# Performance work log

Measured on AMD Instinct MI355X. Metric: run time of the kernel, lower is better.

Reference implementation:

```python
import jax, jax.numpy as jnp
import numpy as np
from math import sqrt

D_MODEL = 1024
N_HEADS = 16
D_V = D_MODEL // N_HEADS
D_FF = 4 * D_MODEL
EPS = 1e-5


def setup_inputs() -> dict:
    key = jax.random.key(0)
    ks = jax.random.split(key, 12)
    N, L = 2, 2048
    s = 0.02
    return {
        'queries': jax.random.normal(ks[0], (N, L, D_MODEL), jnp.float32),
        'keys': jax.random.normal(ks[1], (N, L, D_MODEL), jnp.float32),
        'values': jax.random.normal(ks[2], (N, L, D_MODEL), jnp.float32),
        'mask': jnp.ones((N, 1, 1, L), jnp.int32),
        'fc_w': jax.random.normal(ks[3], (D_MODEL, D_MODEL), jnp.float32) * s,
        'fc_b': jnp.zeros((D_MODEL,), jnp.float32),
        'ln1_g': jnp.ones((D_MODEL,), jnp.float32),
        'ln1_b': jnp.zeros((D_MODEL,), jnp.float32),
        'ff_w1': jax.random.normal(ks[4], (D_MODEL, D_FF), jnp.float32) * s,
        'ff_b1': jnp.zeros((D_FF,), jnp.float32),
        'ff_w2': jax.random.normal(ks[5], (D_FF, D_MODEL), jnp.float32) * s,
        'ff_b2': jnp.zeros((D_MODEL,), jnp.float32),
        'ln2_g': jnp.ones((D_MODEL,), jnp.float32),
        'ln2_b': jnp.zeros((D_MODEL,), jnp.float32),
    }


def layer_norm(x, g, b):
    mu = jnp.mean(x, axis=-1, keepdims=True)
    var = jnp.mean(jnp.square(x - mu), axis=-1, keepdims=True)
    return (x - mu) * jax.lax.rsqrt(var + EPS) * g + b


def reference(queries, keys, values, mask, fc_w, fc_b, ln1_g, ln1_b,
              ff_w1, ff_b1, ff_w2, ff_b2, ln2_g, ln2_b):
    N, Lq, _ = queries.shape
    Lk = keys.shape[1]
    # NOTE: the original module never applies its Q/K/V linear layers; raw
    # inputs are reshaped directly into heads.
    q = queries.reshape(N, Lq, N_HEADS, D_V).transpose(0, 2, 1, 3)  # nhqd
    k = keys.reshape(N, Lk, N_HEADS, D_V)                           # nlhd
    v = values.reshape(N, Lk, N_HEADS, D_V)                         # nlhd
    energy = jnp.einsum('nhqd,nlhd->nhql', q, k)
    energy = jnp.where(mask == 0, -jnp.inf, energy)
    # original scales by sqrt(d_model), not sqrt(d_v)
    attn = jax.nn.softmax(energy / sqrt(D_MODEL), axis=-1)
    out = jnp.einsum('nhql,nlhd->nqhd', attn, v).reshape(N, Lq, D_MODEL)
    attention = out @ fc_w + fc_b
    x1 = layer_norm(attention + queries, ln1_g, ln1_b)
    fc = jax.nn.relu(x1 @ ff_w1 + ff_b1) @ ff_w2 + ff_b2
    x2 = layer_norm(fc + x1, ln2_g, ln2_b)
    return x2
```

## Files before the change

### kernel.cpp

```cpp
#include <hip/hip_runtime.h>
#include <stdint.h>

typedef unsigned short u16;
typedef __bf16 bf16x8 __attribute__((ext_vector_type(8), may_alias));
typedef float f32x4 __attribute__((ext_vector_type(4), may_alias));

typedef void __attribute__((address_space(1))) as1_void;
typedef void __attribute__((address_space(3))) as3_void;

#define MFMA16 __builtin_amdgcn_mfma_f32_16x16x32_bf16

#define SBAR()                                \
    do {                                      \
        asm volatile("" ::: "memory");        \
        __builtin_amdgcn_s_barrier();         \
        asm volatile("" ::: "memory");        \
    } while (0)
#define WAITV(n) asm volatile("s_waitcnt vmcnt(" #n ")" ::: "memory")
#define WAITL0() asm volatile("s_waitcnt lgkmcnt(0)" ::: "memory")

__device__ __forceinline__ void async_copy16(const void* g, void* l) {
    __builtin_amdgcn_global_load_lds((as1_void*)g, (as3_void*)l, 16, 0, 0);
}

__device__ __forceinline__ u16 f2bf(float f) {
    union { float f; unsigned u; } c; c.f = f;
    unsigned u = c.u;
    u += 0x7fffu + ((u >> 16) & 1u);
    return (u16)(u >> 16);
}
__device__ __forceinline__ float bf2f(u16 u) {
    return __uint_as_float((unsigned)u << 16);
}

__global__ __launch_bounds__(256) void prep_all(
    const float* __restrict__ q, u16* __restrict__ qbf, float qscale,
    const float* __restrict__ k, u16* __restrict__ kbf,
    const float* __restrict__ v, u16* __restrict__ vT,
    const float* __restrict__ fcw, u16* __restrict__ fcwT,
    const float* __restrict__ w1, u16* __restrict__ w1T,
    const float* __restrict__ w2, u16* __restrict__ w2T) {
    __shared__ float tile[64][65];
    int g = blockIdx.x;
    int t = threadIdx.x;
    if (g >= 3328) {
        g -= 3328;
        const float* in;
        u16* out;
        float sc;
        if (g < 4096) { in = q; out = qbf; sc = qscale; }
        else { g -= 4096; in = k; out = kbf; sc = 1.0f; }
        size_t i = (size_t)g * 256 + t;
        f32x4 vv = *(const f32x4*)&in[i * 4];
        ushort4 o;
        o.x = f2bf(vv[0] * sc); o.y = f2bf(vv[1] * sc);
        o.z = f2bf(vv[2] * sc); o.w = f2bf(vv[3] * sc);
        *(ushort4*)&out[i * 4] = o;
        return;
    }
    const float* in;
    u16* out;
    int R, C, bx, by, bz = 0;
    if (g < 1024) { in = v; out = vT; R = 2048; C = 1024; bz = g >> 9; g &= 511; bx = g & 15; by = g >> 4; }
    else if (g < 1280) { g -= 1024; in = fcw; out = fcwT; R = 1024; C = 1024; bx = g & 15; by = g >> 4; }
    else if (g < 2304) { g -= 1280; in = w1; out = w1T; R = 1024; C = 4096; bx = g & 63; by = g >> 6; }
    else { g -= 2304; in = w2; out = w2T; R = 4096; C = 1024; bx = g & 15; by = g >> 4; }
    const float* inb = in + (size_t)bz * R * C;
    u16* outb = out + (size_t)bz * R * C;
    int c0 = bx * 64, r0 = by * 64;
    int tr = t >> 4, tc = (t & 15) * 4;
#pragma unroll
    for (int p = 0; p < 4; ++p) {
        int r = tr + p * 16;
        f32x4 vv = *(const f32x4*)&inb[(size_t)(r0 + r) * C + c0 + tc];
        tile[r][tc] = vv[0]; tile[r][tc + 1] = vv[1];
        tile[r][tc + 2] = vv[2]; tile[r][tc + 3] = vv[3];
    }
    __syncthreads();
    int wc = t >> 4, wr = (t & 15) * 4;
#pragma unroll
    for (int p = 0; p < 4; ++p) {
        int cl = wc + p * 16;
        ushort4 o;
        o.x = f2bf(tile[wr + 0][cl]); o.y = f2bf(tile[wr + 1][cl]);
        o.z = f2bf(tile[wr + 2][cl]); o.w = f2bf(tile[wr + 3][cl]);
        *(ushort4*)&outb[(size_t)(c0 + cl) * R + r0 + wr] = o;
    }
}

__global__ __launch_bounds__(256) void flash_attn(
    const u16* __restrict__ Q, const u16* __restrict__ Kb,
    const u16* __restrict__ VT, const int* __restrict__ mask,
    u16* __restrict__ O) {
    __shared__ u16 kls[2][8192];
    __shared__ u16 vls[8192];
    __shared__ u16 pls[8][2048];

    const int bid = blockIdx.x;
    const int qt = bid & 15;
    const int h = (bid >> 4) & 15;
    const int n = bid >> 8;
    const int t = threadIdx.x;
    const int w = t >> 6, lane = t & 63;
    const int m16 = lane & 15, quad = lane >> 4;

    const size_t qrowA = (size_t)(n * 2048 + qt * 128 + w * 16 + m16);
    const size_t qrowB = qrowA + 64;
    bf16x8 qfA0 = *(const bf16x8*)&Q[qrowA * 1024 + h * 64 + quad * 8];
    bf16x8 qfA1 = *(const bf16x8*)&Q[qrowA * 1024 + h * 64 + 32 + quad * 8];
    bf16x8 qfB0 = *(const bf16x8*)&Q[qrowB * 1024 + h * 64 + quad * 8];
    bf16x8 qfB1 = *(const bf16x8*)&Q[qrowB * 1024 + h * 64 + 32 + quad * 8];

    const int* maskn = mask + n * 2048;
    int allones;
    {
        int ok = 1;
#pragma unroll
        for (int i = 0; i < 8; ++i) {
            int4 mv = *(const int4*)&maskn[lane * 32 + i * 4];
            ok &= (mv.x != 0) & (mv.y != 0) & (mv.z != 0) & (mv.w != 0);
        }
        allones = __all(ok);
    }

    f32x4 otA[4] = {}, otB[4] = {};
    f32x4 sumA = {}, sumB = {};

    const u16* Kbase = Kb + (size_t)(n * 2048) * 1024 + h * 64;
    const u16* Vbase = VT + (size_t)(n * 1024 + h * 64) * 2048;
    u16* pwA = &pls[w * 2][0];
    u16* pwB = &pls[w * 2 + 1][0];

#pragma unroll
    for (int i = 0; i < 4; ++i) {
        int e = w * 4 + i;
        async_copy16(&Kbase[(size_t)((e >> 1) * 16 + m16) * 1024 + (e & 1) * 32 + quad * 8],
                     &kls[0][e * 512]);
    }
    __syncthreads();

    for (int kt = 0; kt < 16; ++kt) {
        const u16* kcur = kls[kt & 1];
        if (kt + 1 < 16) {
            u16* knext = kls[(kt + 1) & 1];
#pragma unroll
            for (int i = 0; i < 4; ++i) {
                int e = w * 4 + i;
                async_copy16(&Kbase[(size_t)((kt + 1) * 128 + (e >> 1) * 16 + m16) * 1024 +
                                    (e & 1) * 32 + quad * 8], &knext[e * 512]);
            }
        }
#pragma unroll
        for (int i = 0; i < 4; ++i) {
            int e = w * 4 + i;
            async_copy16(&Vbase[(size_t)((e >> 2) * 16 + m16) * 2048 + kt * 128 +
                                (e & 3) * 32 + quad * 8], &vls[e * 512]);
        }

        f32x4 sA[8] = {}, sB[8] = {};
#pragma unroll
        for (int ct = 0; ct < 8; ++ct) {
            bf16x8 a0 = *(const bf16x8*)&kcur[(ct * 2 + 0) * 512 + lane * 8];
            bf16x8 a1 = *(const bf16x8*)&kcur[(ct * 2 + 1) * 512 + lane * 8];
            sA[ct] = MFMA16(a0, qfA0, sA[ct], 0, 0, 0);
            sA[ct] = MFMA16(a1, qfA1, sA[ct], 0, 0, 0);
            sB[ct] = MFMA16(a0, qfB0, sB[ct], 0, 0, 0);
            sB[ct] = MFMA16(a1, qfB1, sB[ct], 0, 0, 0);
        }

        if (allones) {
#pragma unroll
            for (int ct = 0; ct < 8; ++ct) {
                int c = ct * 2 + (quad >> 1);
                int off = m16 * 128 + (((c ^ m16) & 15) << 3) + (quad & 1) * 4;
                {
                    float p0 = __builtin_amdgcn_exp2f(sA[ct][0]);
                    float p1 = __builtin_amdgcn_exp2f(sA[ct][1]);
                    float p2 = __builtin_amdgcn_exp2f(sA[ct][2]);
                    float p3 = __builtin_amdgcn_exp2f(sA[ct][3]);
                    sumA[0] += p0; sumA[1] += p1; sumA[2] += p2; sumA[3] += p3;
                    unsigned lo = __builtin_amdgcn_perm(__float_as_uint(p1), __float_as_uint(p0), 0x07060302);
                    unsigned hi = __builtin_amdgcn_perm(__float_as_uint(p3), __float_as_uint(p2), 0x07060302);
                    *(uint2*)&pwA[off] = make_uint2(lo, hi);
                }
                {
                    float p0 = __builtin_amdgcn_exp2f(sB[ct][0]);
                    float p1 = __builtin_amdgcn_exp2f(sB[ct][1]);
                    float p2 = __builtin_amdgcn_exp2f(sB[ct][2]);
                    float p3 = __builtin_amdgcn_exp2f(sB[ct][3]);
                    sumB[0] += p0; sumB[1] += p1; sumB[2] += p2; sumB[3] += p3;
                    unsigned lo = __builtin_amdgcn_perm(__float_as_uint(p1), __float_as_uint(p0), 0x07060302);
                    unsigned hi = __builtin_amdgcn_perm(__float_as_uint(p3), __float_as_uint(p2), 0x07060302);
                    *(uint2*)&pwB[off] = make_uint2(lo, hi);
                }
            }
        } else {
#pragma unroll
            for (int ct = 0; ct < 8; ++ct) {
                const int4 mv = *(const int4*)&maskn[kt * 128 + ct * 16 + quad * 4];
                int c = ct * 2 + (quad >> 1);
                int off = m16 * 128 + (((c ^ m16) & 15) << 3) + (quad & 1) * 4;
                {
                    float p0 = __builtin_amdgcn_exp2f(sA[ct][0]) * (mv.x ? 1.f : 0.f);
                    float p1 = __builtin_amdgcn_exp2f(sA[ct][1]) * (mv.y ? 1.f : 0.f);
                    float p2 = __builtin_amdgcn_exp2f(sA[ct][2]) * (mv.z ? 1.f : 0.f);
                    float p3 = __builtin_amdgcn_exp2f(sA[ct][3]) * (mv.w ? 1.f : 0.f);
                    sumA[0] += p0; sumA[1] += p1; sumA[2] += p2; sumA[3] += p3;
                    unsigned lo = __builtin_amdgcn_perm(__float_as_uint(p1), __float_as_uint(p0), 0x07060302);
                    unsigned hi = __builtin_amdgcn_perm(__float_as_uint(p3), __float_as_uint(p2), 0x07060302);
                    *(uint2*)&pwA[off] = make_uint2(lo, hi);
                }
                {
                    float p0 = __builtin_amdgcn_exp2f(sB[ct][0]) * (mv.x ? 1.f : 0.f);
                    float p1 = __builtin_amdgcn_exp2f(sB[ct][1]) * (mv.y ? 1.f : 0.f);
                    float p2 = __builtin_amdgcn_exp2f(sB[ct][2]) * (mv.z ? 1.f : 0.f);
                    float p3 = __builtin_amdgcn_exp2f(sB[ct][3]) * (mv.w ? 1.f : 0.f);
                    sumB[0] += p0; sumB[1] += p1; sumB[2] += p2; sumB[3] += p3;
                    unsigned lo = __builtin_amdgcn_perm(__float_as_uint(p1), __float_as_uint(p0), 0x07060302);
                    unsigned hi = __builtin_amdgcn_perm(__float_as_uint(p3), __float_as_uint(p2), 0x07060302);
                    *(uint2*)&pwB[off] = make_uint2(lo, hi);
                }
            }
        }

        __syncthreads();

        bf16x8 pfA[4], pfB[4];
#pragma unroll
        for (int kc2 = 0; kc2 < 4; ++kc2) {
            int off = m16 * 128 + ((((kc2 * 4 + quad) ^ m16) & 15) << 3);
            pfA[kc2] = *(const bf16x8*)&pwA[off];
            pfB[kc2] = *(const bf16x8*)&pwB[off];
        }
#pragma unroll
        for (int kc2 = 0; kc2 < 4; ++kc2) {
#pragma unroll
            for (int dt = 0; dt < 4; ++dt) {
                bf16x8 vf = *(const bf16x8*)&vls[(dt * 4 + kc2) * 512 + lane * 8];
                otA[dt] = MFMA16(vf, pfA[kc2], otA[dt], 0, 0, 0);
                otB[dt] = MFMA16(vf, pfB[kc2], otB[dt], 0, 0, 0);
            }
        }
        __syncthreads();
    }

    float lA = (sumA[0] + sumA[1]) + (sumA[2] + sumA[3]);
    float lB = (sumB[0] + sumB[1]) + (sumB[2] + sumB[3]);
    lA += __shfl_xor(lA, 16); lA += __shfl_xor(lA, 32);
    lB += __shfl_xor(lB, 16); lB += __shfl_xor(lB, 32);
    float invA = 1.f / fmaxf(lA, 1e-30f);
    float invB = 1.f / fmaxf(lB, 1e-30f);

    const size_t obA = qrowA * 1024 + h * 64;
    const size_t obB = qrowB * 1024 + h * 64;
#pragma unroll
    for (int dt = 0; dt < 4; ++dt) {
        unsigned lo = (unsigned)f2bf(otA[dt][0] * invA) | ((unsigned)f2bf(otA[dt][1] * invA) << 16);
        unsigned hi = (unsigned)f2bf(otA[dt][2] * invA) | ((unsigned)f2bf(otA[dt][3] * invA) << 16);
        *(uint2*)&O[obA + dt * 16 + quad * 4] = make_uint2(lo, hi);
        lo = (unsigned)f2bf(otB[dt][0] * invB) | ((unsigned)f2bf(otB[dt][1] * invB) << 16);
        hi = (unsigned)f2bf(otB[dt][2] * invB) | ((unsigned)f2bf(otB[dt][3] * invB) << 16);
        *(uint2*)&O[obB + dt * 16 + quad * 4] = make_uint2(lo, hi);
    }
}

template <int BM, int BN, int RELU, int OUTBF, int SPLITK>
__global__ __launch_bounds__(256) void gemm_bt(
    const u16* __restrict__ A, const u16* __restrict__ Bt,
    const float* __restrict__ bias, void* __restrict__ Cout,
    void* __restrict__ Cout1, int M, int N, int K) {
    constexpr int MI = BM / 32;
    constexpr int NJ = BN / 32;
    __shared__ u16 sm[2][(BM + BN) * 64];
    const int lane = threadIdx.x & 63;
    const int w = threadIdx.x >> 6;
    const int m16 = lane & 15, quad = lane >> 4;
    const int nBn = N / BN;
    int bid = blockIdx.x;
    int slice = 0;
    if (SPLITK > 1) {
        const int nblk = (M / BM) * nBn;
        slice = bid / nblk;
        bid = bid - slice * nblk;
    }
    const int bm = bid / nBn, bn = bid % nBn;
    const int r2 = w >> 1, c2 = w & 1;
    const int Ks = K / SPLITK;
    const int kOff = slice * Ks;

    const u16* Abase = A + (size_t)(bm * BM + m16) * K + quad * 8;
    const u16* Bbase = Bt + (size_t)(bn * BN + m16) * K + quad * 8;

    auto stage = [&](int buf, int k0) {
        u16* smA = &sm[buf][0];
        u16* smB = smA + BM * 64;
#pragma unroll
        for (int i = 0; i < MI; ++i) {
            int e = w * MI + i;
            async_copy16(&Abase[(size_t)((e >> 1) * 16) * K + k0 + (e & 1) * 32], &smA[e * 512]);
        }
#pragma unroll
        for (int i = 0; i < NJ; ++i) {
            int e = w * NJ + i;
            async_copy16(&Bbase[(size_t)((e >> 1) * 16) * K + k0 + (e & 1) * 32], &smB[e * 512]);
        }
    };

    f32x4 acc[MI][NJ] = {};
    const int nK = Ks >> 6;
    stage(0, kOff);
    __syncthreads();
    for (int kt = 0; kt < nK; ++kt) {
        if (kt + 1 < nK) stage((kt + 1) & 1, kOff + ((kt + 1) << 6));
        const u16* smA = &sm[kt & 1][0];
        const u16* smB = smA + BM * 64;
#pragma unroll
        for (int kc = 0; kc < 2; ++kc) {
            bf16x8 a[MI], b[NJ];
#pragma unroll
            for (int i = 0; i < MI; ++i)
                a[i] = *(const bf16x8*)&smA[((r2 * MI + i) * 2 + kc) * 512 + lane * 8];
#pragma unroll
            for (int j = 0; j < NJ; ++j)
                b[j] = *(const bf16x8*)&smB[((c2 * NJ + j) * 2 + kc) * 512 + lane * 8];
#pragma unroll
            for (int i = 0; i < MI; ++i)
#pragma unroll
                for (int j = 0; j < NJ; ++j)
                    acc[i][j] = MFMA16(a[i], b[j], acc[i][j], 0, 0, 0);
        }
        __syncthreads();
    }
    float bv[NJ];
#pragma unroll
    for (int j = 0; j < NJ; ++j)
        bv[j] = (SPLITK == 1 || slice == 0)
                    ? bias[bn * BN + c2 * (BN / 2) + j * 16 + m16] : 0.f;
    void* Csel = (SPLITK > 1 && slice != 0) ? Cout1 : Cout;
#pragma unroll
    for (int i = 0; i < MI; ++i) {
        int row0 = bm * BM + r2 * (BM / 2) + i * 16 + quad * 4;
#pragma unroll
        for (int j = 0; j < NJ; ++j) {
            int col = bn * BN + c2 * (BN / 2) + j * 16 + m16;
#pragma unroll
            for (int r = 0; r < 4; ++r) {
                float v = acc[i][j][r] + bv[j];
                if (RELU) v = fmaxf(v, 0.f);
                size_t idx = (size_t)(row0 + r) * N + col;
                if (OUTBF) ((u16*)Csel)[idx] = f2bf(v);
                else ((float*)Csel)[idx] = v;
            }
        }
    }
}

template <int RELU, int OUTBF>
__global__ __launch_bounds__(512, 2) void gemm_8ph(
    const u16* __restrict__ A, const u16* __restrict__ Bt,
    const float* __restrict__ bias, void* __restrict__ Cout,
    int M, int N, int K) {
    __shared__ u16 sm[2][2][16384];
    const int t = threadIdx.x;
    const int w = t >> 6, lane = t & 63;
    const int m16 = lane & 15, quad = lane >> 4;
    const int wm = w >> 2, wn = w & 3;
    const int nBn = N >> 8;
    const int bid = blockIdx.x;
    const int bm = bid / nBn, bn = bid % nBn;
    const int nK = K >> 6, nIter = nK >> 1;
    const u16* Abase = A + (size_t)(bm * 256 + m16) * K + quad * 8;
    const u16* Bbase = Bt + (size_t)(bn * 256 + m16) * K + quad * 8;

    auto stage_ht = [&](int kt, int part) {
        if (kt < nK) {
            const u16* base = (part < 2) ? Abase : Bbase;
            u16* lds = &sm[kt & 1][part >> 1][0];
#pragma unroll
            for (int i = 0; i < 2; ++i) {
                int e;
                if (part == 0)      e = i * 16 + w;
                else if (part == 1) e = 8 + i * 16 + w;
                else if (part == 2) e = i * 8 + w;
                else                e = 16 + i * 8 + w;
                async_copy16(&base[(size_t)((e >> 1) * 16) * K + (size_t)kt * 64 + (e & 1) * 32],
                             &lds[e * 512]);
            }
        }
    };
    auto ldsA = [&](int buf, int mf, int kc) {
        return *(const bf16x8*)&sm[buf][0][((wm * 8 + mf) * 2 + kc) * 512 + lane * 8];
    };
    auto ldsB = [&](int buf, int nf, int kc) {
        return *(const bf16x8*)&sm[buf][1][((wn * 4 + nf) * 2 + kc) * 512 + lane * 8];
    };

    f32x4 acc[8][4] = {};
    bf16x8 a0[4][2], a1[4][2], b[4][2];

#define QUAD8(Ar, BO, MO)                                                       \
    do {                                                                        \
        __builtin_amdgcn_s_setprio(1);                                          \
        _Pragma("unroll") for (int mi = 0; mi < 4; ++mi)                        \
            _Pragma("unroll") for (int nj = 0; nj < 2; ++nj)                    \
                _Pragma("unroll") for (int kc = 0; kc < 2; ++kc)                \
                    acc[(MO) + mi][(BO) + nj] =                                 \
                        MFMA16(Ar[mi][kc], b[(BO) + nj][kc],                    \
                               acc[(MO) + mi][(BO) + nj], 0, 0, 0);             \
        __builtin_amdgcn_s_setprio(0);                                          \
    } while (0)

    stage_ht(0, 0); stage_ht(0, 1); stage_ht(0, 2); stage_ht(0, 3);
    stage_ht(1, 0); stage_ht(1, 1); stage_ht(1, 2);
    WAITV(6);
    SBAR();

    for (int it = 0; it < nIter; ++it) {
        const int T1 = 2 * it + 1, T2 = 2 * it + 2, T3 = 2 * it + 3;
        const bool last = (it + 1 == nIter);
#pragma unroll
        for (int mf = 0; mf < 4; ++mf) { a0[mf][0] = ldsA(0, mf, 0); a0[mf][1] = ldsA(0, mf, 1); }
#pragma unroll
        for (int nf = 0; nf < 2; ++nf) { b[nf][0] = ldsB(0, nf, 0); b[nf][1] = ldsB(0, nf, 1); }
        stage_ht(T1, 3);
        SBAR(); WAITL0();
        QUAD8(a0, 0, 0);
        SBAR();
#pragma unroll
        for (int mf = 0; mf < 4; ++mf) { a1[mf][0] = ldsA(0, mf + 4, 0); a1[mf][1] = ldsA(0, mf + 4, 1); }
#pragma unroll
        for (int nf = 0; nf < 2; ++nf) { b[2 + nf][0] = ldsB(0, 2 + nf, 0); b[2 + nf][1] = ldsB(0, 2 + nf, 1); }
        stage_ht(T2, 0);
        SBAR(); WAITL0();
        QUAD8(a0, 2, 0);
        SBAR();
        stage_ht(T2, 1);
        SBAR(); WAITL0();
        QUAD8(a1, 2, 4);
        SBAR();
        stage_ht(T2, 2);
        if (last) { WAITV(0); } else { WAITV(6); }
        SBAR(); WAITL0();
        QUAD8(a1, 0, 4);
        SBAR();
#pragma unroll
        for (int mf = 0; mf < 4; ++mf) { a0[mf][0] = ldsA(1, mf, 0); a0[mf][1] = ldsA(1, mf, 1); }
#pragma unroll
        for (int nf = 0; nf < 2; ++nf) { b[nf][0] = ldsB(1, nf, 0); b[nf][1] = ldsB(1, nf, 1); }
        stage_ht(T2, 3);
        SBAR(); WAITL0();
        QUAD8(a0, 0, 0);
        SBAR();
#pragma unroll
        for (int mf = 0; mf < 4; ++mf) { a1[mf][0] = ldsA(1, mf + 4, 0); a1[mf][1] = ldsA(1, mf + 4, 1); }
#pragma unroll
        for (int nf = 0; nf < 2; ++nf) { b[2 + nf][0] = ldsB(1, 2 + nf, 0); b[2 + nf][1] = ldsB(1, 2 + nf, 1); }
        stage_ht(T3, 0);
        SBAR(); WAITL0();
        QUAD8(a0, 2, 0);
        SBAR();
        stage_ht(T3, 1);
        SBAR(); WAITL0();
        QUAD8(a1, 2, 4);
        SBAR();
        stage_ht(T3, 2);
        if (last) { WAITV(0); } else { WAITV(6); }
        SBAR(); WAITL0();
        QUAD8(a1, 0, 4);
        SBAR();
    }
#undef QUAD8

    float bv[4];
#pragma unroll
    for (int nf = 0; nf < 4; ++nf)
        bv[nf] = bias[bn * 256 + wn * 64 + nf * 16 + m16];
    const int colb = bn * 256 + wn * 64 + m16;
#pragma unroll
    for (int mf = 0; mf < 8; ++mf) {
        const int row0 = bm * 256 + wm * 128 + mf * 16 + quad * 4;
#pragma unroll
        for (int nf = 0; nf < 4; ++nf) {
#pragma unroll
            for (int r = 0; r < 4; ++r) {
                float vv = acc[mf][nf][r] + bv[nf];
                if (RELU) vv = fmaxf(vv, 0.f);
                size_t idx = (size_t)(row0 + r) * N + colb + nf * 16;
                if (OUTBF) ((u16*)Cout)[idx] = f2bf(vv);
                else ((float*)Cout)[idx] = vv;
            }
        }
    }
}

template <int RELU, int OUTBF, int SPLITK>
__global__ __launch_bounds__(512, 2) void gemm_sk(
    const u16* __restrict__ A, const u16* __restrict__ Bt,
    const float* __restrict__ bias,
    void* __restrict__ C0, void* __restrict__ C1,
    int M, int N, int K) {
    __shared__ u16 smA[2][8192];
    __shared__ u16 smB[2][16384];
    const int t = threadIdx.x;
    const int w = t >> 6, lane = t & 63;
    const int m16 = lane & 15, quad = lane >> 4;
    const int wm = w >> 2, wn = w & 3;
    const int nBn = N >> 8;
    const int nblk = (M >> 7) * nBn * SPLITK;
    const int o = blockIdx.x;
    const int v = (o & 7) * (nblk >> 3) + (o >> 3);
    const int gsz = nBn * SPLITK;
    const int bm = v / gsz;
    const int rr = v - bm * gsz;
    const int slice = rr / nBn;
    const int bn = rr - slice * nBn;
    const int Ks = K / SPLITK;
    const int nK = Ks >> 6, nIter = nK >> 1;
    const u16* Abase = A + (size_t)(bm * 128 + m16) * K + slice * Ks + quad * 8;
    const u16* Bbase = Bt + (size_t)(bn * 256 + m16) * K + slice * Ks + quad * 8;

    auto stage_u = [&](int kt, int part) {
        if (kt < nK) {
#pragma unroll
            for (int i = 0; i < 2; ++i) {
                const int idx = i * 8 + w;
                int e;
                const u16* base;
                u16* lds;
                if (part == 0) {
                    e = idx; base = Abase; lds = &smA[kt & 1][0];
                } else {
                    const int rbs = idx >> 1;
                    const int rb = ((rbs >> 1) << 2) | (rbs & 1) | ((part == 2) ? 2 : 0);
                    e = rb * 2 + (idx & 1);
                    base = Bbase; lds = &smB[kt & 1][0];
                }
                async_copy16(&base[(size_t)((e >> 1) * 16) * K + (size_t)kt * 64 + (e & 1) * 32],
                             &lds[e * 512]);
            }
        }
    };
    auto ldsA = [&](int buf, int mf, int kc) {
        return *(const bf16x8*)&smA[buf][((wm * 4 + mf) * 2 + kc) * 512 + lane * 8];
    };
    auto ldsB = [&](int buf, int nf, int kc) {
        return *(const bf16x8*)&smB[buf][((wn * 4 + nf) * 2 + kc) * 512 + lane * 8];
    };

    f32x4 acc[4][4] = {};
    bf16x8 af[4][2], bf[2][2];

#define QUADS(NO)                                                               \
    do {                                                                        \
        __builtin_amdgcn_s_setprio(1);                                          \
        _Pragma("unroll") for (int mi = 0; mi < 4; ++mi)                        \
            _Pragma("unroll") for (int nj = 0; nj < 2; ++nj)                    \
                _Pragma("unroll") for (int kc = 0; kc < 2; ++kc)                \
                    acc[mi][(NO) + nj] =                                        \
                        MFMA16(af[mi][kc], bf[nj][kc],                          \
                               acc[mi][(NO) + nj], 0, 0, 0);                    \
        __builtin_amdgcn_s_setprio(0);                                          \
    } while (0)

    stage_u(0, 0); stage_u(0, 1); stage_u(0, 2);
    stage_u(1, 0); stage_u(1, 1);
    WAITV(4);
    SBAR();

    for (int it = 0; it < nIter; ++it) {
        const int T1 = 2 * it + 1, T2 = 2 * it + 2, T3 = 2 * it + 3;
        const bool last = (it + 1 == nIter);
#pragma unroll
        for (int mf = 0; mf < 4; ++mf) { af[mf][0] = ldsA(0, mf, 0); af[mf][1] = ldsA(0, mf, 1); }
#pragma unroll
        for (int nf = 0; nf < 2; ++nf) { bf[nf][0] = ldsB(0, nf, 0); bf[nf][1] = ldsB(0, nf, 1); }
        stage_u(T1, 2);
        SBAR(); WAITL0();
        QUADS(0);
        SBAR();
#pragma unroll
        for (int nf = 0; nf < 2; ++nf) { bf[nf][0] = ldsB(0, 2 + nf, 0); bf[nf][1] = ldsB(0, 2 + nf, 1); }
        stage_u(T2, 0); stage_u(T2, 1);
        if (last) { WAITV(0); } else { WAITV(4); }
        SBAR(); WAITL0();
        QUADS(2);
        SBAR();
#pragma unroll
        for (int mf = 0; mf < 4; ++mf) { af[mf][0] = ldsA(1, mf, 0); af[mf][1] = ldsA(1, mf, 1); }
#pragma unroll
        for (int nf = 0; nf < 2; ++nf) { bf[nf][0] = ldsB(1, nf, 0); bf[nf][1] = ldsB(1, nf, 1); }
        stage_u(T2, 2);
        SBAR(); WAITL0();
        QUADS(0);
        SBAR();
#pragma unroll
        for (int nf = 0; nf < 2; ++nf) { bf[nf][0] = ldsB(1, 2 + nf, 0); bf[nf][1] = ldsB(1, 2 + nf, 1); }
        stage_u(T3, 0); stage_u(T3, 1);
        if (last) { WAITV(0); } else { WAITV(4); }
        SBAR(); WAITL0();
        QUADS(2);
        SBAR();
    }
#undef QUADS

    float bv[4];
#pragma unroll
    for (int nf = 0; nf < 4; ++nf)
        bv[nf] = (SPLITK == 1 || slice == 0)
                     ? bias[bn * 256 + wn * 64 + nf * 16 + m16] : 0.f;
    void* Csel = (SPLITK > 1 && slice != 0) ? C1 : C0;
    const int colb = bn * 256 + wn * 64 + m16;
#pragma unroll
    for (int mf = 0; mf < 4; ++mf) {
        const int row0 = bm * 128 + wm * 64 + mf * 16 + quad * 4;
#pragma unroll
        for (int nf = 0; nf < 4; ++nf) {
#pragma unroll
            for (int r = 0; r < 4; ++r) {
                float vv = acc[mf][nf][r] + bv[nf];
                if (RELU) vv = fmaxf(vv, 0.f);
                size_t idx = (size_t)(row0 + r) * N + colb + nf * 16;
                if (OUTBF) ((u16*)Csel)[idx] = f2bf(vv);
                else ((float*)Csel)[idx] = vv;
            }
        }
    }
}

template <int RESBF>
__global__ __launch_bounds__(256) void ln_residual(
    const float* __restrict__ x, const float* x2,
    const void* __restrict__ res,
    const float* __restrict__ g, const float* __restrict__ b,
    float* out_f32, u16* __restrict__ out_bf16) {
    __shared__ float smr[8];
    int row = blockIdx.x;
    int t = threadIdx.x;
    f32x4 xv = *(const f32x4*)&x[(size_t)row * 1024 + t * 4];
    f32x4 rv;
    if (RESBF) {
        ushort4 rb = *(const ushort4*)&((const u16*)res)[(size_t)row * 1024 + t * 4];
        rv[0] = bf2f(rb.x); rv[1] = bf2f(rb.y); rv[2] = bf2f(rb.z); rv[3] = bf2f(rb.w);
    } else {
        rv = *(const f32x4*)&((const float*)res)[(size_t)row * 1024 + t * 4];
    }
    xv += rv;
    if (x2) xv += *(const f32x4*)&x2[(size_t)row * 1024 + t * 4];
    float s = xv[0] + xv[1] + xv[2] + xv[3];
    float ss = xv[0] * xv[0] + xv[1] * xv[1] + xv[2] * xv[2] + xv[3] * xv[3];
#pragma unroll
    for (int d = 1; d < 64; d <<= 1) {
        s += __shfl_xor(s, d);
        ss += __shfl_xor(ss, d);
    }
    int w = t >> 6, lane = t & 63;
    if (lane == 0) { smr[w] = s; smr[4 + w] = ss; }
    __syncthreads();
    s = smr[0] + smr[1] + smr[2] + smr[3];
    ss = smr[4] + smr[5] + smr[6] + smr[7];
    float mu = s * (1.f / 1024.f);
    float var = ss * (1.f / 1024.f) - mu * mu;
    float rs = rsqrtf(var + 1e-5f);
    f32x4 gv = *(const f32x4*)&g[t * 4];
    f32x4 bv = *(const f32x4*)&b[t * 4];
    f32x4 y;
#pragma unroll
    for (int i = 0; i < 4; ++i) y[i] = (xv[i] - mu) * rs * gv[i] + bv[i];
    if (out_f32) *(f32x4*)&out_f32[(size_t)row * 1024 + t * 4] = y;
    if (out_bf16) {
        ushort4 o;
        o.x = f2bf(y[0]); o.y = f2bf(y[1]); o.z = f2bf(y[2]); o.w = f2bf(y[3]);
        *(ushort4*)&out_bf16[(size_t)row * 1024 + t * 4] = o;
    }
}

extern "C" void kernel_launch(void* const* d_in, const int* in_sizes, int n_in,
                              void* d_out, int out_size, void* d_ws, size_t ws_size,
                              hipStream_t stream) {
    const float* q = (const float*)d_in[0];
    const float* k = (const float*)d_in[1];
    const float* v = (const float*)d_in[2];
    const int* mask = (const int*)d_in[3];
    const float* fc_b = (const float*)d_in[5];
    const float* ln1_g = (const float*)d_in[6];
    const float* ln1_b = (const float*)d_in[7];
    const float* ff_b1 = (const float*)d_in[9];
    const float* ff_b2 = (const float*)d_in[11];
    const float* ln2_g = (const float*)d_in[12];
    const float* ln2_b = (const float*)d_in[13];
    const float* fc_w = (const float*)d_in[4];
    const float* ff_w1 = (const float*)d_in[8];
    const float* ff_w2 = (const float*)d_in[10];

    char* ws = (char*)d_ws;
    const size_t MB = 1024 * 1024;
    u16* qbf = (u16*)(ws + 0);
    u16* kbf = (u16*)(ws + 8 * MB);
    u16* vT  = (u16*)(ws + 16 * MB);
    u16* ao  = (u16*)(ws + 24 * MB);
    u16* hbuf = (u16*)(ws + 0);
    u16* fcwT = (u16*)(ws + 32 * MB);
    u16* w1T  = (u16*)(ws + 34 * MB);
    u16* w2T  = (u16*)(ws + 42 * MB);
    float* attn_raw = (float*)(ws + 50 * MB);
    float* fc_raw   = (float*)(ws + 50 * MB);
    u16* x1bf   = (u16*)(ws + 82 * MB);
    float* attn_rawB = (float*)(ws + 0);
    float* fcB  = (float*)(ws + 90 * MB);
    const bool big = ws_size >= 106 * MB;

    const float k2 = 0.03125f * 1.44269504088896340736f;

    prep_all<<<11520, 256, 0, stream>>>(q, qbf, k2, k, kbf, v, vT,
                                        fc_w, fcwT, ff_w1, w1T, ff_w2, w2T);

    flash_attn<<<512, 256, 0, stream>>>(qbf, kbf, vT, mask, ao);

    gemm_sk<0, 0, 2><<<256, 512, 0, stream>>>(
        ao, fcwT, fc_b, attn_raw, attn_rawB, 4096, 1024, 1024);
    ln_residual<0><<<4096, 256, 0, stream>>>(attn_raw, attn_rawB, q, ln1_g, ln1_b,
                                             nullptr, x1bf);

    gemm_8ph<1, 1><<<256, 512, 0, stream>>>(
        x1bf, w1T, ff_b1, hbuf, 4096, 4096, 1024);

    if (big) {
        gemm_sk<0, 0, 2><<<256, 512, 0, stream>>>(
            hbuf, w2T, ff_b2, fc_raw, fcB, 4096, 1024, 4096);
        ln_residual<1><<<4096, 256, 0, stream>>>(fc_raw, fcB, x1bf, ln2_g, ln2_b,
                                                 (float*)d_out, (u16*)nullptr);
    } else {
        gemm_bt<64, 128, 0, 0, 1><<<64 * 8, 256, 0, stream>>>(
            hbuf, w2T, ff_b2, fc_raw, nullptr, 4096, 1024, 4096);
        ln_residual<1><<<4096, 256, 0, stream>>>(fc_raw, nullptr, x1bf, ln2_g, ln2_b,
                                                 (float*)d_out, (u16*)nullptr);
    }
}
```

Baseline: 350.9 us.

## Restructure GEMM main loops to overlap LDS reads with MFMA and coalesce bf16 stores

Rewrites the barrier and wait schedule in both GEMM kernels. Fragment reads from LDS are now issued before the MFMA clusters without an immediate lgkmcnt(0) wait, and B fragments are double-registered so the next reads overlap the current math. This removes about half the barriers per iteration. The bf16 epilogue of the large GEMM now stages results through LDS and writes 16-byte coalesced rows instead of scattered 2-byte stores. The main risk is correctness if the reduced waits let LDS buffers be overwritten or read too early.

```diff
diff --git a/kernel.cpp b/kernel.cpp
--- a/kernel.cpp
+++ b/kernel.cpp
@@ -17,7 +17,7 @@
         asm volatile("" ::: "memory");        \
     } while (0)
 #define WAITV(n) asm volatile("s_waitcnt vmcnt(" #n ")" ::: "memory")
-#define WAITL0() asm volatile("s_waitcnt lgkmcnt(0)" ::: "memory")
+#define WAITL(n) asm volatile("s_waitcnt lgkmcnt(" #n ")" ::: "memory")
 
 __device__ __forceinline__ void async_copy16(const void* g, void* l) {
     __builtin_amdgcn_global_load_lds((as1_void*)g, (as3_void*)l, 16, 0, 0);
@@ -396,98 +396,115 @@
     };
 
     f32x4 acc[8][4] = {};
-    bf16x8 a0[4][2], a1[4][2], b[4][2];
-
-#define QUAD8(Ar, BO, MO)                                                       \
+    bf16x8 a0[4][2], a1[4][2], b01[2][2], b23[2][2];
+
+#define RD_A0(buf)                                                              \
+    _Pragma("unroll") for (int mf = 0; mf < 4; ++mf) {                          \
+        a0[mf][0] = ldsA(buf, mf, 0); a0[mf][1] = ldsA(buf, mf, 1); }
+#define RD_A1(buf)                                                              \
+    _Pragma("unroll") for (int mf = 0; mf < 4; ++mf) {                          \
+        a1[mf][0] = ldsA(buf, mf + 4, 0); a1[mf][1] = ldsA(buf, mf + 4, 1); }
+#define RD_B01(buf)                                                             \
+    _Pragma("unroll") for (int nf = 0; nf < 2; ++nf) {                          \
+        b01[nf][0] = ldsB(buf, nf, 0); b01[nf][1] = ldsB(buf, nf, 1); }
+#define RD_B23(buf)                                                             \
+    _Pragma("unroll") for (int nf = 0; nf < 2; ++nf) {                          \
+        b23[nf][0] = ldsB(buf, 2 + nf, 0); b23[nf][1] = ldsB(buf, 2 + nf, 1); }
+#define QUAD8(Ar, Br, MO, NO)                                                   \
     do {                                                                        \
         __builtin_amdgcn_s_setprio(1);                                          \
         _Pragma("unroll") for (int mi = 0; mi < 4; ++mi)                        \
             _Pragma("unroll") for (int nj = 0; nj < 2; ++nj)                    \
                 _Pragma("unroll") for (int kc = 0; kc < 2; ++kc)                \
-                    acc[(MO) + mi][(BO) + nj] =                                 \
-                        MFMA16(Ar[mi][kc], b[(BO) + nj][kc],                    \
-                               acc[(MO) + mi][(BO) + nj], 0, 0, 0);             \
+                    acc[(MO) + mi][(NO) + nj] =                                 \
+                        MFMA16(Ar[mi][kc], Br[nj][kc],                          \
+                               acc[(MO) + mi][(NO) + nj], 0, 0, 0);             \
         __builtin_amdgcn_s_setprio(0);                                          \
     } while (0)
 
     stage_ht(0, 0); stage_ht(0, 1); stage_ht(0, 2); stage_ht(0, 3);
     stage_ht(1, 0); stage_ht(1, 1); stage_ht(1, 2);
-    WAITV(6);
-    SBAR();
 
     for (int it = 0; it < nIter; ++it) {
         const int T1 = 2 * it + 1, T2 = 2 * it + 2, T3 = 2 * it + 3;
         const bool last = (it + 1 == nIter);
-#pragma unroll
-        for (int mf = 0; mf < 4; ++mf) { a0[mf][0] = ldsA(0, mf, 0); a0[mf][1] = ldsA(0, mf, 1); }
-#pragma unroll
-        for (int nf = 0; nf < 2; ++nf) { b[nf][0] = ldsB(0, nf, 0); b[nf][1] = ldsB(0, nf, 1); }
+        WAITV(6);
+        SBAR();
+        RD_A0(0); RD_B01(0);
         stage_ht(T1, 3);
-        SBAR(); WAITL0();
-        QUAD8(a0, 0, 0);
-        SBAR();
-#pragma unroll
-        for (int mf = 0; mf < 4; ++mf) { a1[mf][0] = ldsA(0, mf + 4, 0); a1[mf][1] = ldsA(0, mf + 4, 1); }
-#pragma unroll
-        for (int nf = 0; nf < 2; ++nf) { b[2 + nf][0] = ldsB(0, 2 + nf, 0); b[2 + nf][1] = ldsB(0, 2 + nf, 1); }
+        QUAD8(a0, b01, 0, 0);
+        SBAR();
+        RD_A1(0); RD_B23(0);
         stage_ht(T2, 0);
-        SBAR(); WAITL0();
-        QUAD8(a0, 2, 0);
-        SBAR();
+        QUAD8(a0, b23, 0, 2);
+        SBAR();
+        WAITL(0);
         stage_ht(T2, 1);
-        SBAR(); WAITL0();
-        QUAD8(a1, 2, 4);
+        QUAD8(a1, b23, 4, 2);
         SBAR();
         stage_ht(T2, 2);
+        QUAD8(a1, b01, 4, 0);
         if (last) { WAITV(0); } else { WAITV(6); }
-        SBAR(); WAITL0();
-        QUAD8(a1, 0, 4);
-        SBAR();
-#pragma unroll
-        for (int mf = 0; mf < 4; ++mf) { a0[mf][0] = ldsA(1, mf, 0); a0[mf][1] = ldsA(1, mf, 1); }
-#pragma unroll
-        for (int nf = 0; nf < 2; ++nf) { b[nf][0] = ldsB(1, nf, 0); b[nf][1] = ldsB(1, nf, 1); }
+        SBAR();
+        RD_A0(1); RD_B01(1);
         stage_ht(T2, 3);
-        SBAR(); WAITL0();
-        QUAD8(a0, 0, 0);
-        SBAR();
-#pragma unroll
-        for (int mf = 0; mf < 4; ++mf) { a1[mf][0] = ldsA(1, mf + 4, 0); a1[mf][1] = ldsA(1, mf + 4, 1); }
-#pragma unroll
-        for (int nf = 0; nf < 2; ++nf) { b[2 + nf][0] = ldsB(1, 2 + nf, 0); b[2 + nf][1] = ldsB(1, 2 + nf, 1); }
+        QUAD8(a0, b01, 0, 0);
+        SBAR();
+        RD_A1(1); RD_B23(1);
         stage_ht(T3, 0);
-        SBAR(); WAITL0();
-        QUAD8(a0, 2, 0);
-        SBAR();
+        QUAD8(a0, b23, 0, 2);
+        SBAR();
+        WAITL(0);
         stage_ht(T3, 1);
-        SBAR(); WAITL0();
-        QUAD8(a1, 2, 4);
+        QUAD8(a1, b23, 4, 2);
         SBAR();
         stage_ht(T3, 2);
-        if (last) { WAITV(0); } else { WAITV(6); }
-        SBAR(); WAITL0();
-        QUAD8(a1, 0, 4);
-        SBAR();
+        QUAD8(a1, b01, 4, 0);
     }
 #undef QUAD8
+#undef RD_A0
+#undef RD_A1
+#undef RD_B01
+#undef RD_B23
 
     float bv[4];
 #pragma unroll
     for (int nf = 0; nf < 4; ++nf)
         bv[nf] = bias[bn * 256 + wn * 64 + nf * 16 + m16];
     const int colb = bn * 256 + wn * 64 + m16;
-#pragma unroll
-    for (int mf = 0; mf < 8; ++mf) {
-        const int row0 = bm * 256 + wm * 128 + mf * 16 + quad * 4;
-#pragma unroll
-        for (int nf = 0; nf < 4; ++nf) {
-#pragma unroll
-            for (int r = 0; r < 4; ++r) {
-                float vv = acc[mf][nf][r] + bv[nf];
-                if (RELU) vv = fmaxf(vv, 0.f);
-                size_t idx = (size_t)(row0 + r) * N + colb + nf * 16;
-                if (OUTBF) ((u16*)Cout)[idx] = f2bf(vv);
-                else ((float*)Cout)[idx] = vv;
+    if (OUTBF) {
+        SBAR();
+        u16* myl = &sm[0][0][0] + w * 8192;
+#pragma unroll
+        for (int mf = 0; mf < 8; ++mf)
+#pragma unroll
+            for (int nf = 0; nf < 4; ++nf)
+#pragma unroll
+                for (int r = 0; r < 4; ++r) {
+                    float vv = acc[mf][nf][r] + bv[nf];
+                    if (RELU) vv = fmaxf(vv, 0.f);
+                    myl[(mf * 16 + quad * 4 + r) * 64 + nf * 16 + m16] = f2bf(vv);
+                }
+        const int grow0 = bm * 256 + wm * 128;
+        const int gcol0 = bn * 256 + wn * 64 + (lane & 7) * 8;
+#pragma unroll
+        for (int c = 0; c < 16; ++c) {
+            int row = c * 8 + (lane >> 3);
+            bf16x8 v8 = *(const bf16x8*)&myl[c * 512 + lane * 8];
+            *(bf16x8*)&((u16*)Cout)[(size_t)(grow0 + row) * N + gcol0] = v8;
+        }
+    } else {
+#pragma unroll
+        for (int mf = 0; mf < 8; ++mf) {
+            const int row0 = bm * 256 + wm * 128 + mf * 16 + quad * 4;
+#pragma unroll
+            for (int nf = 0; nf < 4; ++nf) {
+#pragma unroll
+                for (int r = 0; r < 4; ++r) {
+                    float vv = acc[mf][nf][r] + bv[nf];
+                    if (RELU) vv = fmaxf(vv, 0.f);
+                    ((float*)Cout)[(size_t)(row0 + r) * N + colb + nf * 16] = vv;
+                }
             }
         }
     }
@@ -548,60 +565,58 @@
     };
 
     f32x4 acc[4][4] = {};
-    bf16x8 af[4][2], bf[2][2];
-
-#define QUADS(NO)                                                               \
+    bf16x8 af[4][2], al[2][2], be[2][2];
+
+#define RD_AF(buf)                                                              \
+    _Pragma("unroll") for (int mf = 0; mf < 4; ++mf) {                          \
+        af[mf][0] = ldsA(buf, mf, 0); af[mf][1] = ldsA(buf, mf, 1); }
+#define RD_AL(buf)                                                              \
+    _Pragma("unroll") for (int nf = 0; nf < 2; ++nf) {                          \
+        al[nf][0] = ldsB(buf, nf, 0); al[nf][1] = ldsB(buf, nf, 1); }
+#define RD_BE(buf)                                                              \
+    _Pragma("unroll") for (int nf = 0; nf < 2; ++nf) {                          \
+        be[nf][0] = ldsB(buf, 2 + nf, 0); be[nf][1] = ldsB(buf, 2 + nf, 1); }
+#define QUADS(Br, NO)                                                           \
     do {                                                                        \
         __builtin_amdgcn_s_setprio(1);                                          \
         _Pragma("unroll") for (int mi = 0; mi < 4; ++mi)                        \
             _Pragma("unroll") for (int nj = 0; nj < 2; ++nj)                    \
                 _Pragma("unroll") for (int kc = 0; kc < 2; ++kc)                \
                     acc[mi][(NO) + nj] =                                        \
-                        MFMA16(af[mi][kc], bf[nj][kc],                          \
+                        MFMA16(af[mi][kc], Br[nj][kc],                          \
                                acc[mi][(NO) + nj], 0, 0, 0);                    \
         __builtin_amdgcn_s_setprio(0);                                          \
     } while (0)
 
     stage_u(0, 0); stage_u(0, 1); stage_u(0, 2);
     stage_u(1, 0); stage_u(1, 1);
-    WAITV(4);
-    SBAR();
 
     for (int it = 0; it < nIter; ++it) {
         const int T1 = 2 * it + 1, T2 = 2 * it + 2, T3 = 2 * it + 3;
         const bool last = (it + 1 == nIter);
-#pragma unroll
-        for (int mf = 0; mf < 4; ++mf) { af[mf][0] = ldsA(0, mf, 0); af[mf][1] = ldsA(0, mf, 1); }
-#pragma unroll
-        for (int nf = 0; nf < 2; ++nf) { bf[nf][0] = ldsB(0, nf, 0); bf[nf][1] = ldsB(0, nf, 1); }
+        WAITV(4);
+        SBAR();
+        RD_AF(0); RD_AL(0);
         stage_u(T1, 2);
-        SBAR(); WAITL0();
-        QUADS(0);
-        SBAR();
-#pragma unroll
-        for (int nf = 0; nf < 2; ++nf) { bf[nf][0] = ldsB(0, 2 + nf, 0); bf[nf][1] = ldsB(0, 2 + nf, 1); }
+        QUADS(al, 0);
+        SBAR();
+        RD_BE(0);
         stage_u(T2, 0); stage_u(T2, 1);
+        QUADS(be, 2);
         if (last) { WAITV(0); } else { WAITV(4); }
-        SBAR(); WAITL0();
-        QUADS(2);
-        SBAR();
-#pragma unroll
-        for (int mf = 0; mf < 4; ++mf) { af[mf][0] = ldsA(1, mf, 0); af[mf][1] = ldsA(1, mf, 1); }
-#pragma unroll
-        for (int nf = 0; nf < 2; ++nf) { bf[nf][0] = ldsB(1, nf, 0); bf[nf][1] = ldsB(1, nf, 1); }
+        SBAR();
+        RD_AF(1); RD_AL(1);
         stage_u(T2, 2);
-        SBAR(); WAITL0();
-        QUADS(0);
-        SBAR();
-#pragma unroll
-        for (int nf = 0; nf < 2; ++nf) { bf[nf][0] = ldsB(1, 2 + nf, 0); bf[nf][1] = ldsB(1, 2 + nf, 1); }
+        QUADS(al, 0);
+        SBAR();
+        RD_BE(1);
         stage_u(T3, 0); stage_u(T3, 1);
-        if (last) { WAITV(0); } else { WAITV(4); }
-        SBAR(); WAITL0();
-        QUADS(2);
-        SBAR();
+        QUADS(be, 2);
     }
 #undef QUADS
+#undef RD_AF
+#undef RD_AL
+#undef RD_BE
 
     float bv[4];
 #pragma unroll
```

Result: no change. 350.6 us (-0.1%).
